# Performance work log

Hardware: AMD Instinct MI355X
Metric: run time of the kernel (lower is better)

The kernel has to match this reference:

```python
import jax, jax.numpy as jnp
import numpy as np


def _hilbert_envelope(x1d):
    """|analytic signal| of a real 1-D signal, matching scipy.signal.hilbert."""
    N = x1d.shape[0]  # static at trace time
    h = np.zeros(N, dtype=np.float32)
    if N % 2 == 0:
        h[0] = 1.0
        h[N // 2] = 1.0
        h[1:N // 2] = 2.0
    else:
        h[0] = 1.0
        h[1:(N + 1) // 2] = 2.0
    Xf = jnp.fft.fft(x1d)
    analytic = jnp.fft.ifft(Xf * jnp.asarray(h))
    return jnp.abs(analytic)


def setup_inputs() -> dict:
    key = jax.random.key(0)
    B, L, D = 32, 4096, 64
    x = jax.random.normal(key, (B, L, D), dtype=jnp.float32)
    return {"x": x}


def reference(x):
    B, L, D = x.shape
    flat = x.reshape(-1)  # [B*L*D], one long signal as in the original
    up = jnp.clip(flat, 0.0, None)
    down = jnp.clip(-flat, 0.0, None)
    envelope_max = _hilbert_envelope(up).reshape(B, L, D)
    envelope_min = (-_hilbert_envelope(down)).reshape(B, L, D)
    avg_envelope = (envelope_max + envelope_min) * 0.5
    imf = x - avg_envelope
    # torch.std(dim=1, unbiased=True) -> ddof=1 over the time axis
    std_res = jnp.std(imf, axis=1, keepdims=True, ddof=1) + jnp.float32(0.01)
    return imf / std_res, avg_envelope
```

## Files before the change

kernel.cpp:

```cpp
#include <hip/hip_runtime.h>
#include <math.h>

#define NTOT 8388608
#define N1   2048
#define N2   4096
#define BB   32
#define LL   4096
#define DD   64

enum { M_NONE = 0, M_TW = 1, M_SCALE = 4 };

__device__ inline float2 cmul(float2 a, float2 b) {
    return make_float2(a.x*b.x - a.y*b.y, a.x*b.y + a.y*b.x);
}
__device__ inline float2 cmul_conj(float2 a, float2 b) {
    return make_float2(a.x*b.x + a.y*b.y, a.y*b.x - a.x*b.y);
}
__device__ inline float2 cadd(float2 a, float2 b){ return make_float2(a.x+b.x, a.y+b.y); }
__device__ inline float2 csub(float2 a, float2 b){ return make_float2(a.x-b.x, a.y-b.y); }
__device__ inline float2 mul_pi(float2 a){ return make_float2(-a.y, a.x); }
__device__ inline float2 mul_mi(float2 a){ return make_float2(a.y, -a.x); }
__device__ inline int pidx(int a){ return a + (a >> 4); }

template<bool INV>
__device__ inline void dft8(const float2* x, float2* y) {
    const float C = 0.70710678118654752f;
    float2 t0=cadd(x[0],x[4]), t1=cadd(x[1],x[5]), t2=cadd(x[2],x[6]), t3=cadd(x[3],x[7]);
    float2 u0=csub(x[0],x[4]), u1=csub(x[1],x[5]), u2=csub(x[2],x[6]), u3=csub(x[3],x[7]);
    if (!INV) {
        u1 = make_float2(C*(u1.x+u1.y), C*(u1.y-u1.x));
        u2 = mul_mi(u2);
        u3 = make_float2(C*(u3.y-u3.x), -C*(u3.x+u3.y));
    } else {
        u1 = make_float2(C*(u1.x-u1.y), C*(u1.y+u1.x));
        u2 = mul_pi(u2);
        u3 = make_float2(-C*(u3.x+u3.y), C*(u3.x-u3.y));
    }
    {
        float2 s0=cadd(t0,t2), s1=cadd(t1,t3), d0=csub(t0,t2);
        float2 d1 = INV ? mul_pi(csub(t1,t3)) : mul_mi(csub(t1,t3));
        y[0]=cadd(s0,s1); y[4]=csub(s0,s1); y[2]=cadd(d0,d1); y[6]=csub(d0,d1);
    }
    {
        float2 s0=cadd(u0,u2), s1=cadd(u1,u3), d0=csub(u0,u2);
        float2 d1 = INV ? mul_pi(csub(u1,u3)) : mul_mi(csub(u1,u3));
        y[1]=cadd(s0,s1); y[5]=csub(s0,s1); y[3]=cadd(d0,d1); y[7]=csub(d0,d1);
    }
}

__device__ inline void dft8_h0_inv(const float2* x, float2* y) {
    const float C = 0.70710678118654752f;
    float2 u1 = make_float2(C*(x[1].x - x[1].y), C*(x[1].y + x[1].x));
    float2 u2 = mul_pi(x[2]);
    float2 u3 = make_float2(-C*(x[3].x + x[3].y), C*(x[3].x - x[3].y));
    {
        float2 s0=cadd(x[0],x[2]), s1=cadd(x[1],x[3]), d0=csub(x[0],x[2]);
        float2 d1 = mul_pi(csub(x[1],x[3]));
        y[0]=cadd(s0,s1); y[4]=csub(s0,s1); y[2]=cadd(d0,d1); y[6]=csub(d0,d1);
    }
    {
        float2 s0=cadd(x[0],u2), s1=cadd(u1,u3), d0=csub(x[0],u2);
        float2 d1 = mul_pi(csub(u1,u3));
        y[1]=cadd(s0,s1); y[5]=csub(s0,s1); y[3]=cadd(d0,d1); y[7]=csub(d0,d1);
    }
}

template<bool INV>
__device__ inline void dft4(const float2* u, float2* y) {
    float2 s0=cadd(u[0],u[2]), s1=cadd(u[1],u[3]), d0=csub(u[0],u[2]);
    float2 d1 = INV ? mul_pi(csub(u[1],u[3])) : mul_mi(csub(u[1],u[3]));
    y[0]=cadd(s0,s1); y[2]=csub(s0,s1); y[1]=cadd(d0,d1); y[3]=csub(d0,d1);
}

template<bool INV, int SH>
__device__ inline void twiddle8(float2* y, int ps, const float2* __restrict__ T1t) {
    float2 w1 = T1t[(ps << SH) & 4095];
    float2 w2 = cmul(w1, w1);
    float2 w3 = cmul(w2, w1);
    float2 w4 = cmul(w2, w2);
    float2 w5 = cmul(w4, w1);
    float2 w6 = cmul(w3, w3);
    float2 w7 = cmul(w4, w3);
    if (!INV) {
        y[1]=cmul(y[1],w1); y[2]=cmul(y[2],w2); y[3]=cmul(y[3],w3);
        y[4]=cmul(y[4],w4); y[5]=cmul(y[5],w5); y[6]=cmul(y[6],w6); y[7]=cmul(y[7],w7);
    } else {
        y[1]=cmul_conj(y[1],w1); y[2]=cmul_conj(y[2],w2); y[3]=cmul_conj(y[3],w3);
        y[4]=cmul_conj(y[4],w4); y[5]=cmul_conj(y[5],w5); y[6]=cmul_conj(y[6],w6); y[7]=cmul_conj(y[7],w7);
    }
}

__device__ inline float2 wbig(int t, const float2* __restrict__ T1t, const float2* __restrict__ T2t) {
    return cmul(T1t[t >> 11], T2t[t & 2047]);
}

template<bool INV, int MODE>
__global__ __launch_bounds__(512) void fft4096(float2* data,
                                               const float2* __restrict__ T1t,
                                               const float2* __restrict__ T2t) {
    __shared__ float2 S[4352];
    const int t = threadIdx.x;
    const int r = blockIdx.x;
    float2* base = data + (size_t)r * 4096;

    float2 x[8], y[8];
    #pragma unroll
    for (int m = 0; m < 8; ++m) x[m] = base[t + 512*m];

    #pragma unroll
    for (int st = 0; st < 3; ++st) {
        const int s = 1 << (3*st);
        const int q = t & (s - 1);
        const int ps = t - q;
        dft8<INV>(x, y);
        twiddle8<INV, 0>(y, ps, T1t);
        if (st) __syncthreads();
        #pragma unroll
        for (int k = 0; k < 8; ++k) S[pidx(8*ps + q + k*s)] = y[k];
        __syncthreads();
        #pragma unroll
        for (int m = 0; m < 8; ++m) x[m] = S[pidx(t + 512*m)];
    }
    dft8<INV>(x, y);

    if (MODE == M_TW) {
        float2 wb    = wbig(r * t, T1t, T2t);
        float2 wstep = wbig(512 * r, T1t, T2t);
        #pragma unroll
        for (int k = 0; k < 8; ++k) {
            int o = t + 512*k;
            base[o] = INV ? cmul_conj(y[k], wb) : cmul(y[k], wb);
            wb = INV ? cmul_conj(wb, wstep) : cmul(wb, wstep);
        }
    } else {
        #pragma unroll
        for (int k = 0; k < 8; ++k) {
            int o = t + 512*k;
            float2 v = y[k];
            if (MODE == M_SCALE) {
                const float sc = 1.f / 8388608.f;
                v.x *= sc; v.y *= sc;
            }
            base[o] = v;
        }
    }
}

__global__ __launch_bounds__(512) void fftmid(float2* data,
                                              const float2* __restrict__ T1t,
                                              const float2* __restrict__ T2t) {
    __shared__ float2 S2[2][2176];
    const int t    = threadIdx.x & 255;
    const int half = threadIdx.x >> 8;
    const int r    = (blockIdx.x << 1) | half;
    float2* S = S2[half];
    float2* base = data + (size_t)r * 2048;

    float2 x[8], y[8];
    #pragma unroll
    for (int m = 0; m < 8; ++m) x[m] = base[t + 256*m];

    #pragma unroll
    for (int st = 0; st < 3; ++st) {
        const int s = 1 << (3*st);
        const int q = t & (s - 1);
        const int ps = t - q;
        dft8<false>(x, y);
        twiddle8<false, 1>(y, ps, T1t);
        if (st) __syncthreads();
        #pragma unroll
        for (int k = 0; k < 8; ++k) S[pidx(8*ps + q + k*s)] = y[k];
        __syncthreads();
        if (st < 2) {
            #pragma unroll
            for (int m = 0; m < 8; ++m) x[m] = S[pidx(t + 256*m)];
        }
    }
    float2 xa[4], xb[4], ya[4], yb[4];
    #pragma unroll
    for (int m = 0; m < 4; ++m) {
        xa[m] = S[pidx(t + 512*m)];
        xb[m] = S[pidx(t + 256 + 512*m)];
    }
    dft4<false>(xa, ya);
    dft4<false>(xb, yb);
    {
        float2 z[4];
        float h0 = (t == 0 && r == 0) ? 1.f : 2.f;
        z[0] = make_float2(ya[0].x * h0, ya[0].y * h0);
        z[1] = make_float2(yb[0].x * 2.f, yb[0].y * 2.f);
        z[2] = make_float2(ya[1].x * 2.f, ya[1].y * 2.f);
        z[3] = make_float2(yb[1].x * 2.f, yb[1].y * 2.f);
        dft8_h0_inv(z, y);
        if (t == 0 && r == 0) {
            float2 c = ya[2];
            #pragma unroll
            for (int k = 0; k < 8; ++k) {
                if (k & 1) { y[k].x -= c.x; y[k].y -= c.y; }
                else       { y[k].x += c.x; y[k].y += c.y; }
            }
        }
    }
    twiddle8<true, 1>(y, t, T1t);
    __syncthreads();
    #pragma unroll
    for (int k = 0; k < 8; ++k) S[pidx(8*t + k)] = y[k];
    __syncthreads();
    #pragma unroll
    for (int st = 1; st < 3; ++st) {
        const int s = 1 << (3*st);
        const int q = t & (s - 1);
        const int ps = t - q;
        #pragma unroll
        for (int m = 0; m < 8; ++m) x[m] = S[pidx(t + 256*m)];
        dft8<true>(x, y);
        twiddle8<true, 1>(y, ps, T1t);
        __syncthreads();
        #pragma unroll
        for (int k = 0; k < 8; ++k) S[pidx(8*ps + q + k*s)] = y[k];
        __syncthreads();
    }
    #pragma unroll
    for (int m = 0; m < 4; ++m) {
        xa[m] = S[pidx(t + 512*m)];
        xb[m] = S[pidx(t + 256 + 512*m)];
    }
    dft4<true>(xa, ya);
    dft4<true>(xb, yb);
    {
        float2 wka   = wbig(r * t, T1t, T2t);
        float2 w256  = wbig(256 * r, T1t, T2t);
        float2 w512  = cmul(w256, w256);
        float2 wkb   = cmul(wka, w256);
        #pragma unroll
        for (int k = 0; k < 4; ++k) {
            int o = t + 512*k;
            base[o]       = cmul_conj(ya[k], wka);
            base[o + 256] = cmul_conj(yb[k], wkb);
            wka = cmul(wka, w512);
            wkb = cmul(wkb, w512);
        }
    }
}

__global__ __launch_bounds__(256) void k_pre(const float* __restrict__ x, float2* __restrict__ A,
                                             float2* T1, float2* T2) {
    __shared__ float tile[32][33];
    int c0 = blockIdx.x * 32;
    int r0 = blockIdx.y * 32;
    int tx = threadIdx.x, ty = threadIdx.y;
    if (blockIdx.y == 0 && blockIdx.x < 24) {
        int j = blockIdx.x * 256 + ty * 32 + tx;
        if (j < 4096) {
            double ang = -2.0 * M_PI * (double)j / 4096.0;
            T1[j] = make_float2((float)cos(ang), (float)sin(ang));
        } else if (j < 4096 + 2048) {
            int b = j - 4096;
            double ang = -2.0 * M_PI * (double)b / 8388608.0;
            T2[b] = make_float2((float)cos(ang), (float)sin(ang));
        }
    }
    #pragma unroll
    for (int j = 0; j < 32; j += 8)
        tile[ty + j][tx] = x[(size_t)(r0 + ty + j) * N1 + c0 + tx];
    __syncthreads();
    #pragma unroll
    for (int j = 0; j < 32; j += 8) {
        float v = tile[tx][ty + j];
        A[(size_t)(c0 + ty + j) * N2 + r0 + tx] = make_float2(fmaxf(v, 0.f), fmaxf(-v, 0.f));
    }
}

__global__ __launch_bounds__(256) void k_trans(const float2* __restrict__ in, float2* __restrict__ out,
                                               int inCols, int inRows) {
    __shared__ float2 tile[32][33];
    int c0 = blockIdx.x * 32;
    int r0 = blockIdx.y * 32;
    int tx = threadIdx.x, ty = threadIdx.y;
    #pragma unroll
    for (int j = 0; j < 32; j += 8)
        tile[ty + j][tx] = in[(size_t)(r0 + ty + j) * inCols + c0 + tx];
    __syncthreads();
    #pragma unroll
    for (int j = 0; j < 32; j += 8)
        out[(size_t)(c0 + ty + j) * inRows + r0 + tx] = tile[tx][ty + j];
}

__global__ __launch_bounds__(256) void k_post(const float2* __restrict__ A, const float* __restrict__ x,
                                              float* __restrict__ out, float* __restrict__ part) {
    __shared__ float2 tile[32][33];
    __shared__ float red[2][8][32];
    int c0 = blockIdx.x * 32;
    int r0 = blockIdx.y * 32;
    int tx = threadIdx.x, ty = threadIdx.y;
    #pragma unroll
    for (int j = 0; j < 32; j += 8)
        tile[ty + j][tx] = A[(size_t)(r0 + ty + j) * N2 + c0 + tx];
    __syncthreads();
    float s1 = 0.f, s2 = 0.f;
    #pragma unroll
    for (int j = 0; j < 32; j += 8) {
        int n2 = c0 + ty + j;
        int n1 = r0 + tx;
        size_t n = (size_t)n2 * N1 + n1;
        float2 w = tile[tx][ty + j];
        float xv = x[n];
        float up = fmaxf(xv, 0.f);
        float dn = fmaxf(-xv, 0.f);
        float hu = w.y - dn;
        float hd = up - w.x;
        float em = sqrtf(up*up + hu*hu);
        float en = sqrtf(dn*dn + hd*hd);
        float avg = 0.5f * (em - en);
        float imf = xv - avg;
        out[NTOT + n] = avg;
        s1 += imf;
        s2 += imf * imf;
    }
    red[0][ty][tx] = s1;
    red[1][ty][tx] = s2;
    __syncthreads();
    if (ty == 0) {
        #pragma unroll
        for (int e = 1; e < 8; ++e) { s1 += red[0][e][tx]; s2 += red[1][e][tx]; }
        int slot = blockIdx.y * 128 + blockIdx.x;
        part[slot * 32 + tx]          = s1;
        part[262144 + slot * 32 + tx] = s2;
    }
}

__global__ __launch_bounds__(256) void std_final(const float* __restrict__ part, float* __restrict__ scalev) {
    int g = blockIdx.x * 256 + threadIdx.x;
    int b = g >> 6, d = g & 63;
    int dh = d >> 5, dl = d & 31;
    float s1 = 0.f, s2 = 0.f;
    for (int lq = 0; lq < 32; ++lq) {
        int by = lq * 2 + dh;
        #pragma unroll
        for (int ch = 0; ch < 4; ++ch) {
            int slot = by * 128 + b * 4 + ch;
            s1 += part[slot * 32 + dl];
            s2 += part[262144 + slot * 32 + dl];
        }
    }
    float mean = s1 / (float)LL;
    float var  = (s2 - (float)LL * mean * mean) / (float)(LL - 1);
    var = fmaxf(var, 0.f);
    scalev[g] = 1.f / (sqrtf(var) + 0.01f);
}

__global__ __launch_bounds__(256) void imf_final(const float* __restrict__ x, float* __restrict__ out,
                                                 const float* __restrict__ scalev) {
    size_t i = ((size_t)blockIdx.x * 256 + threadIdx.x) * 4;
    float4 xv = *(const float4*)(x + i);
    float4 av = *(const float4*)(out + NTOT + i);
    int b = (int)(i >> 18);
    int d = (int)(i & 63);
    const float* sc = scalev + b * 64;
    float4 v;
    v.x = (xv.x - av.x) * sc[d];
    v.y = (xv.y - av.y) * sc[d + 1];
    v.z = (xv.z - av.z) * sc[d + 2];
    v.w = (xv.w - av.w) * sc[d + 3];
    *(float4*)(out + i) = v;
}

extern "C" void kernel_launch(void* const* d_in, const int* in_sizes, int n_in,
                              void* d_out, int out_size, void* d_ws, size_t ws_size,
                              hipStream_t stream) {
    const float* x = (const float*)d_in[0];
    float* out = (float*)d_out;
    char* w = (char*)d_ws;

    float2* T1     = (float2*)w;
    float2* T2     = (float2*)(w + 32 * 1024);
    float*  scalev = (float*)(w + 48 * 1024);
    float2* A      = (float2*)(w + (1 << 20));
    float2* Bbuf   = (float2*)d_out;
    float*  part   = (float*)d_out;

    hipLaunchKernelGGL(k_pre, dim3(N1/32, N2/32), dim3(32, 8), 0, stream, x, A, T1, T2);
    hipLaunchKernelGGL((fft4096<false, M_TW>), dim3(N1), dim3(512), 0, stream, A, T1, T2);
    hipLaunchKernelGGL(k_trans, dim3(N2/32, N1/32), dim3(32, 8), 0, stream, A, Bbuf, N2, N1);
    hipLaunchKernelGGL(fftmid, dim3(N2/2), dim3(512), 0, stream, Bbuf, T1, T2);
    hipLaunchKernelGGL(k_trans, dim3(N1/32, N2/32), dim3(32, 8), 0, stream, Bbuf, A, N1, N2);
    hipLaunchKernelGGL((fft4096<true, M_SCALE>), dim3(N1), dim3(512), 0, stream, A, T1, T2);

    hipLaunchKernelGGL(k_post, dim3(N2/32, N1/32), dim3(32, 8), 0, stream, A, x, out, part);
    hipLaunchKernelGGL(std_final, dim3(8), dim3(256), 0, stream, part, scalev);
    hipLaunchKernelGGL(imf_final, dim3(NTOT / 4 / 256), dim3(256), 0, stream, x, out, scalev);
}
```

Before: 200.1 us.

## Switch 4096-point FFT to radix-16 with 256 threads per row

Rewrites the 4096-point row FFT from four radix-8 passes with 512 threads to three radix-16 passes with 256 threads, each holding 16 elements in registers. This removes one shared-memory exchange and one barrier per row and lowers the twiddle count. The mid FFT kernel now runs one row per 256-thread block instead of two rows per 512-thread block. The cost is higher register pressure per thread, which may reduce occupancy, and twiddles are now built by chained multiplication from a single table load.

```diff
diff --git a/kernel.cpp b/kernel.cpp
--- a/kernel.cpp
+++ b/kernel.cpp
@@ -45,6 +45,30 @@
         float2 s0=cadd(u0,u2), s1=cadd(u1,u3), d0=csub(u0,u2);
         float2 d1 = INV ? mul_pi(csub(u1,u3)) : mul_mi(csub(u1,u3));
         y[1]=cadd(s0,s1); y[5]=csub(s0,s1); y[3]=cadd(d0,d1); y[7]=csub(d0,d1);
+    }
+}
+
+template<bool INV>
+__device__ inline void dft16(const float2* x, float2* y) {
+    const float C  = 0.70710678118654752f;
+    const float c1 = 0.92387953251128674f;
+    const float s1 = 0.38268343236508977f;
+    float2 e[8], o[8], E[8], O[8];
+    #pragma unroll
+    for (int m = 0; m < 8; ++m) { e[m] = x[2*m]; o[m] = x[2*m+1]; }
+    dft8<INV>(e, E);
+    dft8<INV>(o, O);
+    O[1] = cmul(O[1], make_float2( c1, INV ?  s1 : -s1));
+    O[2] = cmul(O[2], make_float2(  C, INV ?   C : -C ));
+    O[3] = cmul(O[3], make_float2( s1, INV ?  c1 : -c1));
+    O[4] = INV ? mul_pi(O[4]) : mul_mi(O[4]);
+    O[5] = cmul(O[5], make_float2(-s1, INV ?  c1 : -c1));
+    O[6] = cmul(O[6], make_float2( -C, INV ?   C : -C ));
+    O[7] = cmul(O[7], make_float2(-c1, INV ?  s1 : -s1));
+    #pragma unroll
+    for (int k = 0; k < 8; ++k) {
+        y[k]     = cadd(E[k], O[k]);
+        y[k + 8] = csub(E[k], O[k]);
     }
 }
 
@@ -90,12 +114,35 @@
     }
 }
 
+template<bool INV>
+__device__ inline void twiddle16(float2* y, int ps, const float2* __restrict__ T1t) {
+    float2 w[16];
+    w[1] = T1t[ps & 4095];
+    w[2] = cmul(w[1], w[1]);
+    w[3] = cmul(w[2], w[1]);
+    w[4] = cmul(w[2], w[2]);
+    w[5] = cmul(w[4], w[1]);
+    w[6] = cmul(w[3], w[3]);
+    w[7] = cmul(w[4], w[3]);
+    w[8] = cmul(w[4], w[4]);
+    w[9] = cmul(w[8], w[1]);
+    w[10]= cmul(w[5], w[5]);
+    w[11]= cmul(w[8], w[3]);
+    w[12]= cmul(w[6], w[6]);
+    w[13]= cmul(w[8], w[5]);
+    w[14]= cmul(w[7], w[7]);
+    w[15]= cmul(w[8], w[7]);
+    #pragma unroll
+    for (int k = 1; k < 16; ++k)
+        y[k] = INV ? cmul_conj(y[k], w[k]) : cmul(y[k], w[k]);
+}
+
 __device__ inline float2 wbig(int t, const float2* __restrict__ T1t, const float2* __restrict__ T2t) {
     return cmul(T1t[t >> 11], T2t[t & 2047]);
 }
 
 template<bool INV, int MODE>
-__global__ __launch_bounds__(512) void fft4096(float2* data,
+__global__ __launch_bounds__(256) void fft4096(float2* data,
                                                const float2* __restrict__ T1t,
                                                const float2* __restrict__ T2t) {
     __shared__ float2 S[4352];
@@ -103,39 +150,45 @@
     const int r = blockIdx.x;
     float2* base = data + (size_t)r * 4096;
 
-    float2 x[8], y[8];
-    #pragma unroll
-    for (int m = 0; m < 8; ++m) x[m] = base[t + 512*m];
-
-    #pragma unroll
-    for (int st = 0; st < 3; ++st) {
-        const int s = 1 << (3*st);
-        const int q = t & (s - 1);
-        const int ps = t - q;
-        dft8<INV>(x, y);
-        twiddle8<INV, 0>(y, ps, T1t);
-        if (st) __syncthreads();
-        #pragma unroll
-        for (int k = 0; k < 8; ++k) S[pidx(8*ps + q + k*s)] = y[k];
+    float2 x[16], y[16];
+    #pragma unroll
+    for (int m = 0; m < 16; ++m) x[m] = base[t + 256*m];
+
+    dft16<INV>(x, y);
+    twiddle16<INV>(y, t, T1t);
+    #pragma unroll
+    for (int k = 0; k < 16; ++k) S[pidx(16*t + k)] = y[k];
+    __syncthreads();
+    #pragma unroll
+    for (int m = 0; m < 16; ++m) x[m] = S[pidx(t + 256*m)];
+
+    dft16<INV>(x, y);
+    {
+        const int q = t & 15, ps = t - q;
+        twiddle16<INV>(y, ps, T1t);
         __syncthreads();
         #pragma unroll
-        for (int m = 0; m < 8; ++m) x[m] = S[pidx(t + 512*m)];
-    }
-    dft8<INV>(x, y);
+        for (int k = 0; k < 16; ++k) S[pidx(16*ps + q + 16*k)] = y[k];
+    }
+    __syncthreads();
+    #pragma unroll
+    for (int m = 0; m < 16; ++m) x[m] = S[pidx(t + 256*m)];
+
+    dft16<INV>(x, y);
 
     if (MODE == M_TW) {
         float2 wb    = wbig(r * t, T1t, T2t);
-        float2 wstep = wbig(512 * r, T1t, T2t);
-        #pragma unroll
-        for (int k = 0; k < 8; ++k) {
-            int o = t + 512*k;
+        float2 wstep = wbig(256 * r, T1t, T2t);
+        #pragma unroll
+        for (int k = 0; k < 16; ++k) {
+            int o = t + 256*k;
             base[o] = INV ? cmul_conj(y[k], wb) : cmul(y[k], wb);
             wb = INV ? cmul_conj(wb, wstep) : cmul(wb, wstep);
         }
     } else {
         #pragma unroll
-        for (int k = 0; k < 8; ++k) {
-            int o = t + 512*k;
+        for (int k = 0; k < 16; ++k) {
+            int o = t + 256*k;
             float2 v = y[k];
             if (MODE == M_SCALE) {
                 const float sc = 1.f / 8388608.f;
@@ -146,14 +199,12 @@
     }
 }
 
-__global__ __launch_bounds__(512) void fftmid(float2* data,
+__global__ __launch_bounds__(256) void fftmid(float2* data,
                                               const float2* __restrict__ T1t,
                                               const float2* __restrict__ T2t) {
-    __shared__ float2 S2[2][2176];
-    const int t    = threadIdx.x & 255;
-    const int half = threadIdx.x >> 8;
-    const int r    = (blockIdx.x << 1) | half;
-    float2* S = S2[half];
+    __shared__ float2 S[2176];
+    const int t = threadIdx.x;
+    const int r = blockIdx.x;
     float2* base = data + (size_t)r * 2048;
 
     float2 x[8], y[8];
@@ -380,11 +431,11 @@
     float*  part   = (float*)d_out;
 
     hipLaunchKernelGGL(k_pre, dim3(N1/32, N2/32), dim3(32, 8), 0, stream, x, A, T1, T2);
-    hipLaunchKernelGGL((fft4096<false, M_TW>), dim3(N1), dim3(512), 0, stream, A, T1, T2);
+    hipLaunchKernelGGL((fft4096<false, M_TW>), dim3(N1), dim3(256), 0, stream, A, T1, T2);
     hipLaunchKernelGGL(k_trans, dim3(N2/32, N1/32), dim3(32, 8), 0, stream, A, Bbuf, N2, N1);
-    hipLaunchKernelGGL(fftmid, dim3(N2/2), dim3(512), 0, stream, Bbuf, T1, T2);
+    hipLaunchKernelGGL(fftmid, dim3(N2), dim3(256), 0, stream, Bbuf, T1, T2);
     hipLaunchKernelGGL(k_trans, dim3(N1/32, N2/32), dim3(32, 8), 0, stream, Bbuf, A, N1, N2);
-    hipLaunchKernelGGL((fft4096<true, M_SCALE>), dim3(N1), dim3(512), 0, stream, A, T1, T2);
+    hipLaunchKernelGGL((fft4096<true, M_SCALE>), dim3(N1), dim3(256), 0, stream, A, T1, T2);
 
     hipLaunchKernelGGL(k_post, dim3(N2/32, N1/32), dim3(32, 8), 0, stream, A, x, out, part);
     hipLaunchKernelGGL(std_final, dim3(8), dim3(256), 0, stream, part, scalev);
```

New measurement: 197.6 us. No clear change (-1.3%).
